# Kernel tuning notes

Hardware: AMD Instinct MI355X
Metric: run time of the kernel (lower is better)

The kernel has to match this reference:

```python
import jax, jax.numpy as jnp
import numpy as np

B, N, K, D = 8, 32768, 128, 64
TAU, ITERS, EPS = 1.0, 10, 1e-8


def setup_inputs() -> dict:
    key = jax.random.key(0)
    k1, k2, k3 = jax.random.split(key, 3)
    xyz = jax.random.normal(k1, (B, 3, N), dtype=jnp.float32)
    feats = jax.random.normal(k2, (B, D, N), dtype=jnp.float32)
    o_scores = jax.random.uniform(k3, (B, N), dtype=jnp.float32)
    return {"xyz": xyz, "feats": feats, "o_scores": o_scores}


def _sq_dist(x, c):
    # x: (B,N,3), c: (B,K,3) -> (B,N,K) squared euclidean distance
    x2 = jnp.sum(x * x, axis=-1, keepdims=True)          # (B,N,1)
    c2 = jnp.sum(c * c, axis=-1)[:, None, :]              # (B,1,K)
    xc = jnp.einsum('bnd,bkd->bnk', x, c)                 # (B,N,K)
    return x2 + c2 - 2.0 * xc


def _wkeans_plus(x, f, s, n_clusters, iters, tau):
    # x: (B,N,3) points, f: (B,N,D) features, s: (B,N) soft weights
    n = x.shape[1]
    # deterministic init: evenly strided points as initial centroids
    init_idx = jnp.arange(n_clusters) * (n // n_clusters)
    centers = x[:, init_idx, :]                           # (B,K,3)
    w = s[..., None]                                      # (B,N,1)
    s_sum = jnp.sum(s, axis=1, keepdims=True) + EPS       # (B,1)
    gamma = None
    denom = None
    for _ in range(iters):
        d = _sq_dist(x, centers)                          # (B,N,K)
        gamma = jax.nn.softmax(-d / tau, axis=-1) * w     # (B,N,K) weighted soft assignment
        denom = jnp.sum(gamma, axis=1) + EPS              # (B,K)
        centers = jnp.einsum('bnk,bnd->bkd', gamma, x) / denom[..., None]
    pi = jnp.sum(gamma, axis=1) / s_sum                   # (B,K) mixing weights
    node_feats = jnp.einsum('bnk,bnd->bkd', gamma, f) / denom[..., None]  # (B,K,D)
    return gamma, pi, centers, node_feats


def reference(xyz, feats, o_scores):
    x = jnp.swapaxes(xyz, -1, -2)    # (B,N,3)
    f = jnp.swapaxes(feats, -1, -2)  # (B,N,D)
    gamma, pi, node_xyz, node_feats = _wkeans_plus(x, f, o_scores, K, ITERS, TAU)
    return gamma, pi, node_xyz, node_feats
```

## Files before the change

### kernel.cpp

```cpp
#include <hip/hip_runtime.h>
#include <hip/hip_bf16.h>

typedef __attribute__((ext_vector_type(8))) short short8;
typedef __attribute__((ext_vector_type(4))) float f32x4;

#define BB 8
#define NN 32768
#define KK 128
#define DD 64
#define TAU 1.0f
#define ITERS 10
#define EPSV 1e-8f
#define JPARTS 128

#define G_SZ   ((size_t)BB * NN * KK)
#define PI_OFF (G_SZ)
#define XY_OFF (PI_OFF + (size_t)BB * KK)
#define NF_OUT (XY_OFF + (size_t)BB * KK * 3)

#define SLICE_F (BB * KK * 4)
#define SS_OFF  ((ITERS + 1) * SLICE_F)
#define HDR_F   (SS_OFF + 16)
#define PART_OFF HDR_F
#define PART_F  ((size_t)JPARTS * BB * KK * DD)
#define WS_NEED_BYTES  ((PART_OFF + PART_F) * 4)

__device__ __forceinline__ unsigned pk2(float a, float b) {
    __hip_bfloat162 h = __float22bfloat162_rn(make_float2(a, b));
    unsigned u; __builtin_memcpy(&u, &h, 4); return u;
}

__global__ __launch_bounds__(256) void prep_kernel(const float* __restrict__ xyz,
                                                   const float* __restrict__ sc,
                                                   float* __restrict__ ws) {
    int b = blockIdx.x, tid = threadIdx.x, wave = tid >> 6, lane = tid & 63;
    const float* S = sc + (size_t)b * NN;
    float sum = 0.f;
    for (int i = tid; i < NN; i += 256) sum += S[i];
    #pragma unroll
    for (int m = 1; m <= 32; m <<= 1) sum += __shfl_xor(sum, m, 64);
    __shared__ float red[4];
    if (lane == 0) red[wave] = sum;
    __syncthreads();
    if (tid == 0) ws[SS_OFF + b] = red[0] + red[1] + red[2] + red[3] + EPSV;
    if (tid < KK) {
        const float* X = xyz + (size_t)b * 3 * NN;
        int i0 = tid * (NN / KK);
        ((float4*)ws)[b * KK + tid] =
            make_float4(X[i0], X[NN + i0], X[2 * NN + i0], 1.0f);
    }
}

template <bool LAST>
__global__ __launch_bounds__(256) void assign_kernel(
    const float* __restrict__ xyz, const float* __restrict__ sc,
    const float4* __restrict__ accIn,
    float* __restrict__ accOut,
    float* __restrict__ gamma_out)
{
    __shared__ float4 cLds[KK];
    __shared__ float4 wLds[256];
    __shared__ float  accW[4][512];

    const int b = blockIdx.y, blk = blockIdx.x;
    const int tid = threadIdx.x, wave = tid >> 6, lane = tid & 63;

    const float* X = xyz + (size_t)b * 3 * NN;
    const float* S = sc + (size_t)b * NN;

    const int n = blk * 256 + tid;
    const float px = X[n], py = X[NN + n], pz = X[2 * NN + n], ps = S[n];

    if (tid < KK) {
        float4 a = accIn[b * KK + tid];
        float denom = a.w + EPSV;
        float cx = a.x / denom, cy = a.y / denom, cz = a.z / denom;
        cLds[tid] = make_float4(2.f * cx / TAU, 2.f * cy / TAU, 2.f * cz / TAU,
                                -(cx * cx + cy * cy + cz * cz) / TAU);
    }
    __syncthreads();

    float l0 = 0.f, l1 = 0.f;
    #pragma unroll 8
    for (int k = 0; k < KK; k += 2) {
        float4 ca = cLds[k], cb = cLds[k + 1];
        l0 += __expf(fmaf(px, ca.x, fmaf(py, ca.y, fmaf(pz, ca.z, ca.w))));
        l1 += __expf(fmaf(px, cb.x, fmaf(py, cb.y, fmaf(pz, cb.z, cb.w))));
    }
    wLds[tid] = make_float4(px, py, pz, ps / (l0 + l1));
    __syncthreads();

    const float4 c0 = cLds[lane];
    const float4 c1 = cLds[lane + 64];
    float ax0 = 0, ay0 = 0, az0 = 0, aw0 = 0;
    float ax1 = 0, ay1 = 0, az1 = 0, aw1 = 0;
    float* grow = gamma_out + ((size_t)b * NN + blk * 256 + (wave << 6)) * KK + lane;

    #pragma unroll 4
    for (int j = 0; j < 64; ++j) {
        float4 P = wLds[(wave << 6) | j];
        float g0 = __expf(fmaf(P.x, c0.x, fmaf(P.y, c0.y, fmaf(P.z, c0.z, c0.w)))) * P.w;
        float g1 = __expf(fmaf(P.x, c1.x, fmaf(P.y, c1.y, fmaf(P.z, c1.z, c1.w)))) * P.w;
        if (LAST) {
            grow[(size_t)j * KK] = g0;
            grow[(size_t)j * KK + 64] = g1;
        }
        ax0 = fmaf(g0, P.x, ax0); ay0 = fmaf(g0, P.y, ay0);
        az0 = fmaf(g0, P.z, az0); aw0 += g0;
        ax1 = fmaf(g1, P.x, ax1); ay1 = fmaf(g1, P.y, ay1);
        az1 = fmaf(g1, P.z, az1); aw1 += g1;
    }

    ((float4*)accW[wave])[lane]      = make_float4(ax0, ay0, az0, aw0);
    ((float4*)accW[wave])[lane + 64] = make_float4(ax1, ay1, az1, aw1);
    __syncthreads();
    float v0 = accW[0][tid]       + accW[1][tid]       + accW[2][tid]       + accW[3][tid];
    float v1 = accW[0][tid + 256] + accW[1][tid + 256] + accW[2][tid + 256] + accW[3][tid + 256];
    float* ag = accOut + b * (KK * 4);
    atomicAdd(ag + tid, v0);
    atomicAdd(ag + tid + 256, v1);
}

__global__ void final_kernel(const float* __restrict__ ws, float* __restrict__ out) {
    int b = blockIdx.x, k = threadIdx.x;
    float4 a = ((const float4*)(ws + ITERS * SLICE_F))[b * KK + k];
    float denom = a.w + EPSV;
    float* oxyz = out + XY_OFF + (size_t)(b * KK + k) * 3;
    oxyz[0] = a.x / denom; oxyz[1] = a.y / denom; oxyz[2] = a.z / denom;
    out[PI_OFF + b * KK + k] = a.w / ws[SS_OFF + b];
}

__global__ __launch_bounds__(256) void nf_mfma2(const float* __restrict__ gamma,
                                                const float* __restrict__ feats,
                                                float* __restrict__ dst) {
    __shared__ unsigned short gT[KK * 40];
    const int b = blockIdx.y, part = blockIdx.x;
    const int tid = threadIdx.x, wave = tid >> 6, lane = tid & 63;
    const int r = lane & 15, hi = lane >> 4;
    const int p = tid & 15, q0 = tid >> 4;

    f32x4 acc[2][4];
    #pragma unroll
    for (int kt = 0; kt < 2; kt++)
        #pragma unroll
        for (int dt = 0; dt < 4; dt++) acc[kt][dt] = (f32x4){0.f, 0.f, 0.f, 0.f};

    const float* gb = gamma + (size_t)b * NN * KK + (size_t)part * 256 * KK;
    const float* fb = feats + (size_t)b * DD * NN;
    const int n0 = part * 256;

    for (int ch = 0; ch < 8; ++ch) {
        const float* gr0 = gb + (size_t)(ch * 32 + 2 * p) * KK;
        const float* gr1 = gr0 + KK;
        unsigned* rowd = (unsigned*)gT;
        #pragma unroll
        for (int s = 0; s < 2; ++s) {
            int q = q0 + 16 * s;
            float4 x = *(const float4*)(gr0 + 4 * q);
            float4 y = *(const float4*)(gr1 + 4 * q);
            rowd[(4 * q + 0) * 20 + p] = pk2(x.x, y.x);
            rowd[(4 * q + 1) * 20 + p] = pk2(x.y, y.y);
            rowd[(4 * q + 2) * 20 + p] = pk2(x.z, y.z);
            rowd[(4 * q + 3) * 20 + p] = pk2(x.w, y.w);
        }
        __syncthreads();

        const unsigned short* a0p = gT + (wave * 32 + r) * 40 + hi * 8;
        short8 a0 = *(const short8*)a0p;
        short8 a1 = *(const short8*)(a0p + 16 * 40);
        const int nn = n0 + ch * 32 + hi * 8;
        #pragma unroll
        for (int dt = 0; dt < 4; ++dt) {
            const float* fr = fb + (size_t)(dt * 16 + r) * NN + nn;
            float4 x = *(const float4*)fr;
            float4 y = *(const float4*)(fr + 4);
            union { unsigned u[4]; short8 s; } bu;
            bu.u[0] = pk2(x.x, x.y); bu.u[1] = pk2(x.z, x.w);
            bu.u[2] = pk2(y.x, y.y); bu.u[3] = pk2(y.z, y.w);
            acc[0][dt] = __builtin_amdgcn_mfma_f32_16x16x32_bf16(a0, bu.s, acc[0][dt], 0, 0, 0);
            acc[1][dt] = __builtin_amdgcn_mfma_f32_16x16x32_bf16(a1, bu.s, acc[1][dt], 0, 0, 0);
        }
        __syncthreads();
    }

    float* pdst = dst + ((size_t)(b * JPARTS + part)) * (KK * DD) + (size_t)(wave * 32) * DD;
    #pragma unroll
    for (int kt = 0; kt < 2; kt++)
        #pragma unroll
        for (int dt = 0; dt < 4; dt++)
            #pragma unroll
            for (int rr = 0; rr < 4; rr++)
                pdst[(kt * 16 + hi * 4 + rr) * DD + dt * 16 + r] = acc[kt][dt][rr];
}

__global__ __launch_bounds__(256) void nf_compute_atomic(const float* __restrict__ gamma,
                                                         const float* __restrict__ feats,
                                                         float* __restrict__ dst) {
    __shared__ float gLds[32 * 128];
    __shared__ float fLds[64 * 33];
    const int b = blockIdx.y, part = blockIdx.x, tid = threadIdx.x;
    const int kq = (tid & 15) * 8, dg = (tid >> 4) * 4;
    float acc[8][4];
    #pragma unroll
    for (int i = 0; i < 8; i++)
        #pragma unroll
        for (int u = 0; u < 4; u++) acc[i][u] = 0.f;
    const float* gb = gamma + (size_t)b * NN * KK + (size_t)part * (NN / JPARTS) * KK;
    const float* fb = feats + (size_t)b * DD * NN + part * (NN / JPARTS);
    for (int ch = 0; ch < (NN / JPARTS) / 32; ++ch) {
        const float4* gs = (const float4*)(gb + (size_t)ch * 32 * KK);
        #pragma unroll
        for (int i = 0; i < 4; i++) ((float4*)gLds)[tid + i * 256] = gs[tid + i * 256];
        #pragma unroll
        for (int i = 0; i < 2; i++) {
            int idx = tid + i * 256;
            int d = idx >> 3, c4 = (idx & 7) * 4;
            float4 fv = *(const float4*)(fb + (size_t)d * NN + ch * 32 + c4);
            float* fr = &fLds[d * 33 + c4];
            fr[0] = fv.x; fr[1] = fv.y; fr[2] = fv.z; fr[3] = fv.w;
        }
        __syncthreads();
        #pragma unroll 4
        for (int nl = 0; nl < 32; ++nl) {
            float4 g0 = *(const float4*)&gLds[nl * 128 + kq];
            float4 g1 = *(const float4*)&gLds[nl * 128 + kq + 4];
            float fv[4];
            #pragma unroll
            for (int u = 0; u < 4; u++) fv[u] = fLds[(dg + u) * 33 + nl];
            float gk[8] = {g0.x, g0.y, g0.z, g0.w, g1.x, g1.y, g1.z, g1.w};
            #pragma unroll
            for (int i = 0; i < 8; i++)
                #pragma unroll
                for (int u = 0; u < 4; u++)
                    acc[i][u] = fmaf(gk[i], fv[u], acc[i][u]);
        }
        __syncthreads();
    }
    float* nf = dst + (size_t)b * KK * DD;
    #pragma unroll
    for (int i = 0; i < 8; i++)
        #pragma unroll
        for (int u = 0; u < 4; u++)
            atomicAdd(&nf[(kq + i) * DD + dg + u], acc[i][u]);
}

__global__ __launch_bounds__(256) void nf_reduce(const float* __restrict__ ws,
                                                 float* __restrict__ out) {
    int idx = blockIdx.x * 256 + threadIdx.x;
    int b = idx >> 13, e = idx & 8191;
    const float* p = ws + PART_OFF + (size_t)b * JPARTS * (KK * DD) + e;
    float sum = 0.f;
    #pragma unroll 8
    for (int j = 0; j < JPARTS; ++j) sum += p[(size_t)j * (KK * DD)];
    int k = e >> 6;
    float denom = ws[ITERS * SLICE_F + (b * KK + k) * 4 + 3] + EPSV;
    out[NF_OUT + idx] = sum / denom;
}

__global__ __launch_bounds__(256) void nf_finalize(const float* __restrict__ ws,
                                                   float* __restrict__ out) {
    int idx = blockIdx.x * 256 + threadIdx.x;
    int bk = idx / DD;
    float denom = ws[ITERS * SLICE_F + bk * 4 + 3] + EPSV;
    out[NF_OUT + idx] = out[NF_OUT + idx] / denom;
}

extern "C" void kernel_launch(void* const* d_in, const int* in_sizes, int n_in,
                              void* d_out, int out_size, void* d_ws, size_t ws_size,
                              hipStream_t stream) {
    const float* xyz = (const float*)d_in[0];
    const float* feats = (const float*)d_in[1];
    const float* sc = (const float*)d_in[2];
    float* out = (float*)d_out;
    float* ws = (float*)d_ws;

    hipMemsetAsync(ws, 0, (size_t)HDR_F * sizeof(float), stream);
    prep_kernel<<<BB, 256, 0, stream>>>(xyz, sc, ws);

    for (int it = 0; it < ITERS - 1; it++) {
        assign_kernel<false><<<dim3(128, BB), 256, 0, stream>>>(
            xyz, sc, (const float4*)(ws + it * SLICE_F),
            ws + (it + 1) * SLICE_F, out);
    }
    assign_kernel<true><<<dim3(128, BB), 256, 0, stream>>>(
        xyz, sc, (const float4*)(ws + (ITERS - 1) * SLICE_F),
        ws + ITERS * SLICE_F, out);

    final_kernel<<<BB, KK, 0, stream>>>(ws, out);

    if (ws_size >= WS_NEED_BYTES) {
        nf_mfma2<<<dim3(JPARTS, BB), 256, 0, stream>>>(out, feats, ws + PART_OFF);
        nf_reduce<<<256, 256, 0, stream>>>(ws, out);
    } else {
        hipMemsetAsync(out + NF_OUT, 0, (size_t)BB * KK * DD * sizeof(float), stream);
        nf_compute_atomic<<<dim3(JPARTS, BB), 256, 0, stream>>>(out, feats, out + NF_OUT);
        nf_finalize<<<256, 256, 0, stream>>>(ws, out);
    }
}
```

Measured before the change: 301.2 us.

## Replace LDS broadcasts with readlane and process two points per thread in assign kernel

The assign kernel no longer stages centroids and weighted points in shared memory. Each wave computes centroids in registers and broadcasts them with readlane. Each thread now handles two points, which halves the grid to 64 blocks per batch and cuts two __syncthreads barriers. The intent is to remove LDS traffic and barrier stalls, at the cost of more scalar readlane instructions and fewer blocks (512 total) to fill the GPU.

```diff
diff --git a/kernel.cpp b/kernel.cpp
--- a/kernel.cpp
+++ b/kernel.cpp
@@ -28,6 +28,9 @@
 __device__ __forceinline__ unsigned pk2(float a, float b) {
     __hip_bfloat162 h = __float22bfloat162_rn(make_float2(a, b));
     unsigned u; __builtin_memcpy(&u, &h, 4); return u;
+}
+__device__ __forceinline__ float rdl(float v, int l) {
+    return __int_as_float(__builtin_amdgcn_readlane(__float_as_int(v), l));
 }
 
 __global__ __launch_bounds__(256) void prep_kernel(const float* __restrict__ xyz,
@@ -58,9 +61,7 @@
     float* __restrict__ accOut,
     float* __restrict__ gamma_out)
 {
-    __shared__ float4 cLds[KK];
-    __shared__ float4 wLds[256];
-    __shared__ float  accW[4][512];
+    __shared__ float accW[4][512];
 
     const int b = blockIdx.y, blk = blockIdx.x;
     const int tid = threadIdx.x, wave = tid >> 6, lane = tid & 63;
@@ -68,47 +69,66 @@
     const float* X = xyz + (size_t)b * 3 * NN;
     const float* S = sc + (size_t)b * NN;
 
-    const int n = blk * 256 + tid;
-    const float px = X[n], py = X[NN + n], pz = X[2 * NN + n], ps = S[n];
-
-    if (tid < KK) {
-        float4 a = accIn[b * KK + tid];
-        float denom = a.w + EPSV;
-        float cx = a.x / denom, cy = a.y / denom, cz = a.z / denom;
-        cLds[tid] = make_float4(2.f * cx / TAU, 2.f * cy / TAU, 2.f * cz / TAU,
-                                -(cx * cx + cy * cy + cz * cz) / TAU);
-    }
-    __syncthreads();
+    const int n0 = blk * 512 + (wave << 7) + lane;
+    const float px0 = X[n0],      py0 = X[NN + n0],      pz0 = X[2 * NN + n0],      ps0 = S[n0];
+    const float px1 = X[n0 + 64], py1 = X[NN + n0 + 64], pz1 = X[2 * NN + n0 + 64], ps1 = S[n0 + 64];
+
+    float4 a0 = accIn[b * KK + lane];
+    float4 a1 = accIn[b * KK + 64 + lane];
+    float d0 = a0.w + EPSV, d1 = a1.w + EPSV;
+    float cx0 = a0.x / d0, cy0 = a0.y / d0, cz0 = a0.z / d0;
+    float cx1 = a1.x / d1, cy1 = a1.y / d1, cz1 = a1.z / d1;
+    const float4 c0 = make_float4(2.f * cx0 / TAU, 2.f * cy0 / TAU, 2.f * cz0 / TAU,
+                                  -(cx0 * cx0 + cy0 * cy0 + cz0 * cz0) / TAU);
+    const float4 c1 = make_float4(2.f * cx1 / TAU, 2.f * cy1 / TAU, 2.f * cz1 / TAU,
+                                  -(cx1 * cx1 + cy1 * cy1 + cz1 * cz1) / TAU);
 
     float l0 = 0.f, l1 = 0.f;
     #pragma unroll 8
-    for (int k = 0; k < KK; k += 2) {
-        float4 ca = cLds[k], cb = cLds[k + 1];
-        l0 += __expf(fmaf(px, ca.x, fmaf(py, ca.y, fmaf(pz, ca.z, ca.w))));
-        l1 += __expf(fmaf(px, cb.x, fmaf(py, cb.y, fmaf(pz, cb.z, cb.w))));
-    }
-    wLds[tid] = make_float4(px, py, pz, ps / (l0 + l1));
-    __syncthreads();
-
-    const float4 c0 = cLds[lane];
-    const float4 c1 = cLds[lane + 64];
+    for (int k = 0; k < 64; ++k) {
+        float cx = rdl(c0.x, k), cy = rdl(c0.y, k), cz = rdl(c0.z, k), cw = rdl(c0.w, k);
+        l0 += __expf(fmaf(px0, cx, fmaf(py0, cy, fmaf(pz0, cz, cw))));
+        l1 += __expf(fmaf(px1, cx, fmaf(py1, cy, fmaf(pz1, cz, cw))));
+    }
+    #pragma unroll 8
+    for (int k = 0; k < 64; ++k) {
+        float cx = rdl(c1.x, k), cy = rdl(c1.y, k), cz = rdl(c1.z, k), cw = rdl(c1.w, k);
+        l0 += __expf(fmaf(px0, cx, fmaf(py0, cy, fmaf(pz0, cz, cw))));
+        l1 += __expf(fmaf(px1, cx, fmaf(py1, cy, fmaf(pz1, cz, cw))));
+    }
+    const float w0 = ps0 / l0, w1 = ps1 / l1;
+
     float ax0 = 0, ay0 = 0, az0 = 0, aw0 = 0;
     float ax1 = 0, ay1 = 0, az1 = 0, aw1 = 0;
-    float* grow = gamma_out + ((size_t)b * NN + blk * 256 + (wave << 6)) * KK + lane;
-
-    #pragma unroll 4
+    float* grow = gamma_out + ((size_t)b * NN + blk * 512 + (wave << 7)) * KK + lane;
+
+    #pragma unroll 8
     for (int j = 0; j < 64; ++j) {
-        float4 P = wLds[(wave << 6) | j];
-        float g0 = __expf(fmaf(P.x, c0.x, fmaf(P.y, c0.y, fmaf(P.z, c0.z, c0.w)))) * P.w;
-        float g1 = __expf(fmaf(P.x, c1.x, fmaf(P.y, c1.y, fmaf(P.z, c1.z, c1.w)))) * P.w;
+        float qx = rdl(px0, j), qy = rdl(py0, j), qz = rdl(pz0, j), qw = rdl(w0, j);
+        float g0 = __expf(fmaf(qx, c0.x, fmaf(qy, c0.y, fmaf(qz, c0.z, c0.w)))) * qw;
+        float g1 = __expf(fmaf(qx, c1.x, fmaf(qy, c1.y, fmaf(qz, c1.z, c1.w)))) * qw;
         if (LAST) {
             grow[(size_t)j * KK] = g0;
             grow[(size_t)j * KK + 64] = g1;
         }
-        ax0 = fmaf(g0, P.x, ax0); ay0 = fmaf(g0, P.y, ay0);
-        az0 = fmaf(g0, P.z, az0); aw0 += g0;
-        ax1 = fmaf(g1, P.x, ax1); ay1 = fmaf(g1, P.y, ay1);
-        az1 = fmaf(g1, P.z, az1); aw1 += g1;
+        ax0 = fmaf(g0, qx, ax0); ay0 = fmaf(g0, qy, ay0);
+        az0 = fmaf(g0, qz, az0); aw0 += g0;
+        ax1 = fmaf(g1, qx, ax1); ay1 = fmaf(g1, qy, ay1);
+        az1 = fmaf(g1, qz, az1); aw1 += g1;
+    }
+    #pragma unroll 8
+    for (int j = 0; j < 64; ++j) {
+        float qx = rdl(px1, j), qy = rdl(py1, j), qz = rdl(pz1, j), qw = rdl(w1, j);
+        float g0 = __expf(fmaf(qx, c0.x, fmaf(qy, c0.y, fmaf(qz, c0.z, c0.w)))) * qw;
+        float g1 = __expf(fmaf(qx, c1.x, fmaf(qy, c1.y, fmaf(qz, c1.z, c1.w)))) * qw;
+        if (LAST) {
+            grow[(size_t)(j + 64) * KK] = g0;
+            grow[(size_t)(j + 64) * KK + 64] = g1;
+        }
+        ax0 = fmaf(g0, qx, ax0); ay0 = fmaf(g0, qy, ay0);
+        az0 = fmaf(g0, qz, az0); aw0 += g0;
+        ax1 = fmaf(g1, qx, ax1); ay1 = fmaf(g1, qy, ay1);
+        az1 = fmaf(g1, qz, az1); aw1 += g1;
     }
 
     ((float4*)accW[wave])[lane]      = make_float4(ax0, ay0, az0, aw0);
@@ -278,11 +298,11 @@
     prep_kernel<<<BB, 256, 0, stream>>>(xyz, sc, ws);
 
     for (int it = 0; it < ITERS - 1; it++) {
-        assign_kernel<false><<<dim3(128, BB), 256, 0, stream>>>(
+        assign_kernel<false><<<dim3(64, BB), 256, 0, stream>>>(
             xyz, sc, (const float4*)(ws + it * SLICE_F),
             ws + (it + 1) * SLICE_F, out);
     }
-    assign_kernel<true><<<dim3(128, BB), 256, 0, stream>>>(
+    assign_kernel<true><<<dim3(64, BB), 256, 0, stream>>>(
         xyz, sc, (const float4*)(ws + (ITERS - 1) * SLICE_F),
         ws + ITERS * SLICE_F, out);
 
```

Result: slower. 358.5 us (+19.0%).
